# Kernel tuning notes

Hardware: AMD Instinct MI355X
Metric: run time of the kernel (lower is better)

The kernel has to match this reference:

```python
import jax, jax.numpy as jnp
import numpy as np

# ---- static part graph (matches torch.nonzero row-major edge order) ----
ADJ = np.array([[0,1,0,0,0,0],
                [1,0,1,1,1,1],
                [0,1,0,0,0,0],
                [0,1,0,0,0,0],
                [0,1,0,0,0,1],
                [0,1,0,0,1,0]], dtype=np.int64)
EDGES = [(int(u), int(v)) for u, v in np.argwhere(ADJ)]  # 12 edges
P = ADJ.shape[0]                 # 6 part nodes (cls_p - 1)
PART_LIST = [[] for _ in range(P)]
for u, v in EDGES:
    PART_LIST[v].append(u)
DEG = [len(l) for l in PART_LIST]  # [1,5,1,1,2,2], sum = 12
CLS_P = P + 1
IN_DIM, HID = 256, 10
N, H, W = 4, 64, 64


def spatial_coords(h, w):
    """[8,h,w] coord features, same as generate_spatial_batch (vectorized)."""
    ws = np.arange(w, dtype=np.float32); hs = np.arange(h, dtype=np.float32)
    xmin = ws / w * 2 - 1; xmax = (ws + 1) / w * 2 - 1; xctr = (xmin + xmax) / 2
    ymin = hs / h * 2 - 1; ymax = (hs + 1) / h * 2 - 1; yctr = (ymin + ymax) / 2
    f = np.zeros((h, w, 8), np.float32)
    f[..., 0] = xmin[None, :]; f[..., 1] = ymin[:, None]
    f[..., 2] = xmax[None, :]; f[..., 3] = ymax[:, None]
    f[..., 4] = xctr[None, :]; f[..., 5] = yctr[:, None]
    f[..., 6] = 1.0 / w;       f[..., 7] = 1.0 / h
    return jnp.asarray(f.transpose(2, 0, 1))


def conv1x1(x, w, b=None):
    y = jnp.einsum('nchw,oc->nohw', x, w)
    return y if b is None else y + b[None, :, None, None]


def conv3x3(x, w):
    return jax.lax.conv_general_dilated(x, w, (1, 1), 'SAME',
                                        dimension_numbers=('NCHW', 'OIHW', 'NCHW'))


def bn(x, g, b, eps=1e-5):
    mu = x.mean((0, 2, 3), keepdims=True)
    var = ((x - mu) ** 2).mean((0, 2, 3), keepdims=True)
    return (x - mu) * jax.lax.rsqrt(var + eps) * g[None, :, None, None] + b[None, :, None, None]


def setup_inputs() -> dict:
    key = jax.random.key(0)
    ks = jax.random.split(key, 16)
    s = 0.05
    return {
        'xp':      jax.random.normal(ks[0], (N, IN_DIM, H, W), jnp.float32),
        'p_nodes': jax.random.normal(ks[1], (CLS_P, N, HID, H, W), jnp.float32),
        'p_atts':  jax.random.normal(ks[2], (CLS_P, N, 1, H, W), jnp.float32),
        'W_key':  jax.random.normal(ks[3], (64, IN_DIM + 8), jnp.float32) * s,
        'b_key':  jnp.zeros((64,), jnp.float32),
        'W_q':    jax.random.normal(ks[4], (64, IN_DIM + 8), jnp.float32) * s,
        'b_q':    jnp.zeros((64,), jnp.float32),
        'W_att':  jax.random.normal(ks[5], (sum(DEG), IN_DIM + 1), jnp.float32) * s,
        'b_att':  jnp.zeros((sum(DEG),), jnp.float32),
        'W_proj': jax.random.normal(ks[6], (HID, IN_DIM), jnp.float32) * s,
        'g_proj': jnp.ones((HID,), jnp.float32),
        'bt_proj': jnp.zeros((HID,), jnp.float32),
        'W_rel1': jax.random.normal(ks[7], (2 * HID, 2 * HID, 3, 3), jnp.float32) * s,
        'g_rel1': jnp.ones((2 * HID,), jnp.float32),
        'bt_rel1': jnp.zeros((2 * HID,), jnp.float32),
        'W_rel2': jax.random.normal(ks[8], (HID, 2 * HID), jnp.float32) * s,
        'b_rel2': jnp.zeros((HID,), jnp.float32),
        'Wg':    jax.random.normal(ks[9], (P, 2, 2 * HID), jnp.float32) * s,
        'bg':    jnp.zeros((P, 2), jnp.float32),
        'Wc':    jax.random.normal(ks[10], (P, HID, 2 * HID), jnp.float32) * s,
        'g_can': jnp.ones((P, HID), jnp.float32),
        'bt_can': jnp.zeros((P, HID), jnp.float32),
    }


def reference(xp, p_nodes, p_atts,
              W_key, b_key, W_q, b_q, W_att, b_att,
              W_proj, g_proj, bt_proj, W_rel1, g_rel1, bt_rel1, W_rel2, b_rel2,
              Wg, bg, Wc, g_can, bt_can):
    n, c, h, w = xp.shape
    L = h * w
    coord = jnp.broadcast_to(spatial_coords(h, w), (n, 8, h, w))

    # ---- Dep_Context (vectorized over the P part nodes) ----
    feat = jnp.concatenate([xp, coord], axis=1)                 # [n, 264, h, w]
    key_f = conv1x1(feat, W_key, b_key).reshape(n, 64, L)       # [n, 64, L]
    p_att = p_atts[1:]                                          # [P, n, 1, h, w]
    norm = jax.nn.softmax(p_att.reshape(P, n, L), axis=-1)      # [P, n, L]
    hu_c = jnp.einsum('ncl,pnl->pnc', xp.reshape(n, c, L), norm)       # [P, n, 256]
    co_c = jnp.einsum('ncl,pnl->pnc', coord.reshape(n, 8, L), norm)    # [P, n, 8]
    cen = jnp.concatenate([hu_c, co_c], axis=-1)                # [P, n, 264]
    q = jnp.einsum('pnf,of->pno', cen, W_q) + b_q               # [P, n, 64]
    energy = jnp.einsum('pno,nol->pnl', q, key_f)               # [P, n, L]
    attn = jax.nn.sigmoid(energy).reshape(P, n, 1, h, w)
    one_m = 1.0 - p_att
    F_dep_att = attn * one_m                                    # [P, n, 1, h, w]
    F_dep = attn * xp[None] * one_m                             # [P, n, 256, h, w]

    # ---- Contexture attention heads (per-node conv, deg_i output channels) ----
    att_logits, att_soft = [], []
    off = 0
    for i in range(P):
        d = DEG[i]
        inp = jnp.concatenate([F_dep_att[i], xp], axis=1)       # [n, 257, h, w]
        logit = conv1x1(inp, W_att[off:off + d], b_att[off:off + d])
        att_logits.append(logit)
        att_soft.append(jax.nn.softmax(logit, axis=1))
        off += d

    # ---- Dependency messages per edge ----
    def dependency(hv, hu_ctx, dep_att):
        msg = jax.nn.relu(bn(conv1x1(hu_ctx * dep_att, W_proj), g_proj, bt_proj))
        x = jnp.concatenate([msg, hv], axis=1)                  # [n, 20, h, w]
        x = jax.nn.relu(bn(conv3x3(x, W_rel1), g_rel1, bt_rel1))
        return jax.nn.sigmoid(conv1x1(x, W_rel2, b_rel2))       # [n, 10, h, w]

    msgs = [None] * P
    for u, v in EDGES:
        ch = PART_LIST[u].index(v)
        # NB: original code indexes p_node_list with the raw edge target v
        m = dependency(p_nodes[v], F_dep[u], att_soft[u][:, ch:ch + 1])
        msgs[v] = m if msgs[v] is None else msgs[v] + m

    # ---- ConvGRU node updates ----
    new_nodes = [p_nodes[0]]
    for i in range(P):
        h_cur, msg = p_nodes[i + 1], msgs[i]
        gates = conv1x1(jnp.concatenate([msg, h_cur], axis=1), Wg[i], bg[i])
        r = jax.nn.sigmoid(gates[:, 0:1]); z = jax.nn.sigmoid(gates[:, 1:2])
        cnm = conv1x1(jnp.concatenate([msg, r * h_cur], axis=1), Wc[i])
        cnm = jax.nn.leaky_relu(bn(cnm, g_can[i], bt_can[i]), 0.01)  # InPlaceABNSync default
        new_nodes.append((1.0 - z) * h_cur + z * cnm)

    xp_new = jnp.stack(new_nodes)                               # [cls_p, n, 10, h, w]
    fdep_att = jnp.concatenate(att_logits, axis=1)              # [n, 12, h, w]
    return xp_new, fdep_att
```

## Files before the change

### kernel.cpp

```cpp
#include <hip/hip_runtime.h>
#include <math.h>

#define L 4096

__constant__ int c_EV[12]   = {1,0,2,3,4,5,1,1,1,5,1,4};
__constant__ int c_INOFF[7] = {0,1,6,7,8,10,12};
__constant__ int c_INE[12]  = {1, 0,6,7,8,10, 2, 3, 4,11, 5,9};

__device__ inline float sigmf(float x){ return 1.f/(1.f+expf(-x)); }

__global__ __launch_bounds__(256) void k_softmax_norm(const float* __restrict__ p_atts,
                                                      float* __restrict__ norm,
                                                      const float* __restrict__ W_rel1,
                                                      float* __restrict__ wt2){
  int tid = threadIdx.x;
  if (blockIdx.x == 24){
    for (int i = tid; i < 3600; i += 256){
      int co = i % 10; int t = i / 10;
      int k = t % 9; t /= 9;
      int h = t & 1; int ci = t >> 1;
      wt2[i] = W_rel1[(((h * 10 + co) * 20) + ci) * 9 + k];
    }
    return;
  }
  int pn = blockIdx.x;
  const float* src = p_atts + (size_t)(pn + 4) * L;
  float* dst = norm + (size_t)pn * L;
  __shared__ float red[256];
  float m = -1e30f;
  for (int l = tid; l < L; l += 256) m = fmaxf(m, src[l]);
  red[tid] = m; __syncthreads();
  for (int s = 128; s; s >>= 1){ if (tid < s) red[tid] = fmaxf(red[tid], red[tid+s]); __syncthreads(); }
  m = red[0]; __syncthreads();
  float sum = 0.f;
  for (int l = tid; l < L; l += 256) sum += expf(src[l] - m);
  red[tid] = sum; __syncthreads();
  for (int s = 128; s; s >>= 1){ if (tid < s) red[tid] += red[tid+s]; __syncthreads(); }
  float inv = 1.f / red[0];
  for (int l = tid; l < L; l += 256) dst[l] = expf(src[l] - m) * inv;
}

__device__ inline float coord_feat(int cc, int l){
  int h = l >> 6, w = l & 63;
  const float s = 2.f / 64.f;
  switch (cc){
    case 0: return w * s - 1.f;
    case 1: return h * s - 1.f;
    case 2: return (w + 1) * s - 1.f;
    case 3: return (h + 1) * s - 1.f;
    case 4: return (w + 0.5f) * s - 1.f;
    case 5: return (h + 0.5f) * s - 1.f;
    default: return 1.f / 64.f;
  }
}

__global__ __launch_bounds__(256) void k_centroid(const float* __restrict__ xp,
                                                  const float* __restrict__ norm,
                                                  float* __restrict__ cen){
  int c0 = blockIdx.x;
  int c1 = c0 + 132;
  int n = blockIdx.y;
  int tid = threadIdx.x;
  float acc[2][6];
#pragma unroll
  for (int q = 0; q < 2; q++)
#pragma unroll
    for (int p = 0; p < 6; p++) acc[q][p] = 0.f;
  const float* nr0 = norm + (size_t)n * L;
  const float* xr0 = xp + ((size_t)n * 256 + c0) * L;
  const float* xr1 = (c1 < 256) ? xp + ((size_t)n * 256 + c1) * L : nullptr;
  int cc1 = c1 - 256;
  for (int l = tid; l < L; l += 256){
    float nv[6];
#pragma unroll
    for (int p = 0; p < 6; p++) nv[p] = nr0[(size_t)p * 4 * L + l];
    float x0 = xr0[l];
    float x1 = (c1 < 256) ? xr1[l] : coord_feat(cc1, l);
#pragma unroll
    for (int p = 0; p < 6; p++){
      acc[0][p] = fmaf(x0, nv[p], acc[0][p]);
      acc[1][p] = fmaf(x1, nv[p], acc[1][p]);
    }
  }
#pragma unroll
  for (int q = 0; q < 2; q++)
#pragma unroll
    for (int p = 0; p < 6; p++){
      for (int off = 32; off; off >>= 1) acc[q][p] += __shfl_xor(acc[q][p], off, 64);
    }
  __shared__ float red[2][6][4];
  int wv = tid >> 6;
  if ((tid & 63) == 0){
#pragma unroll
    for (int q = 0; q < 2; q++)
#pragma unroll
      for (int p = 0; p < 6; p++) red[q][p][wv] = acc[q][p];
  }
  __syncthreads();
  if (tid < 12){
    int q = tid / 6, p = tid % 6;
    float s = red[q][p][0] + red[q][p][1] + red[q][p][2] + red[q][p][3];
    cen[(size_t)(p * 4 + n) * 264 + (q ? c1 : c0)] = s;
  }
}

__global__ __launch_bounds__(256) void k_qk(const float* __restrict__ cen,
                                            const float* __restrict__ W_q, const float* __restrict__ b_q,
                                            const float* __restrict__ W_key, const float* __restrict__ b_key,
                                            float* __restrict__ qk, float* __restrict__ qb){
  int pn = blockIdx.x;
  int tid = threadIdx.x;
  __shared__ float cen_s[264];
  __shared__ float qs[64];
  __shared__ float part[256];
  for (int i = tid; i < 264; i += 256) cen_s[i] = cen[(size_t)pn * 264 + i];
  __syncthreads();
  int o = tid >> 2, pr = tid & 3;
  {
    float a = 0.f;
    int f0 = pr * 66;
    for (int j = 0; j < 66; j++){ int f = f0 + j; a = fmaf(cen_s[f], W_q[o * 264 + f], a); }
    part[tid] = a;
  }
  __syncthreads();
  if (pr == 0) qs[o] = part[tid] + part[tid + 1] + part[tid + 2] + part[tid + 3] + b_q[o];
  __syncthreads();
  for (int c = tid; c < 264; c += 256){
    float a = 0.f;
    for (int oo = 0; oo < 64; oo++) a = fmaf(qs[oo], W_key[oo * 264 + c], a);
    qk[(size_t)pn * 264 + c] = a;
  }
  if (tid < 64) part[tid] = qs[tid] * b_key[tid];
  __syncthreads();
  if (tid == 0){
    float a = 0.f;
    for (int oo = 0; oo < 64; oo++) a += part[oo];
    qb[pn] = a;
  }
}

__global__ __launch_bounds__(256) void k_pixel(const float* __restrict__ xp,
                                              const float* __restrict__ p_atts,
                                              const float* __restrict__ W_att, const float* __restrict__ b_att,
                                              const float* __restrict__ W_proj,
                                              const float* __restrict__ qk, const float* __restrict__ qb,
                                              float* __restrict__ out_fdep,
                                              float* __restrict__ s_edge,
                                              float* __restrict__ proj_x,
                                              float* __restrict__ mpart){
  __shared__ float s_watt[256 * 12];
  __shared__ float s_wproj[256 * 12];
  __shared__ float s_qk[256 * 8];
  __shared__ float s_qkt[48];
  __shared__ float pacc[4][28][64];
  __shared__ float w0[12], ba[12], qbs[6];
  int n = blockIdx.y;
  int tid = threadIdx.x;
  int wv = tid >> 6, w = tid & 63;
  int l = blockIdx.x * 64 + w;
  for (int i = tid; i < 256 * 12; i += 256){ int c = i / 12, j = i % 12; s_watt[i] = W_att[j * 257 + 1 + c]; }
  for (int i = tid; i < 256 * 12; i += 256){ int c = i / 12, k = i % 12; s_wproj[i] = (k < 10) ? W_proj[k * 256 + c] : 0.f; }
  for (int i = tid; i < 256 * 8; i += 256){ int c = i >> 3, p = i & 7; s_qk[i] = (p < 6) ? qk[((size_t)(p * 4 + n)) * 264 + c] : 0.f; }
  if (tid < 48){ int p = tid >> 3, cc = tid & 7; s_qkt[tid] = qk[((size_t)(p * 4 + n)) * 264 + 256 + cc]; }
  if (tid < 12){ w0[tid] = W_att[tid * 257]; ba[tid] = b_att[tid]; }
  if (tid < 6) qbs[tid] = qb[tid * 4 + n];
  __syncthreads();

  float a[32];
#pragma unroll
  for (int f = 0; f < 32; f++) a[f] = 0.f;
  const float* xpn = xp + (size_t)n * 256 * L + l;
  int c0 = wv * 64;
#pragma unroll 2
  for (int cc = 0; cc < 64; cc++){
    int c = c0 + cc;
    float xv = xpn[(size_t)c * L];
    float4 wa0 = *(const float4*)(s_watt + c * 12);
    float4 wa1 = *(const float4*)(s_watt + c * 12 + 4);
    float4 wa2 = *(const float4*)(s_watt + c * 12 + 8);
    float4 wp0 = *(const float4*)(s_wproj + c * 12);
    float4 wp1 = *(const float4*)(s_wproj + c * 12 + 4);
    float4 wp2 = *(const float4*)(s_wproj + c * 12 + 8);
    float4 wq0 = *(const float4*)(s_qk + c * 8);
    float4 wq1 = *(const float4*)(s_qk + c * 8 + 4);
    a[0]  = fmaf(xv, wa0.x, a[0]);  a[1]  = fmaf(xv, wa0.y, a[1]);
    a[2]  = fmaf(xv, wa0.z, a[2]);  a[3]  = fmaf(xv, wa0.w, a[3]);
    a[4]  = fmaf(xv, wa1.x, a[4]);  a[5]  = fmaf(xv, wa1.y, a[5]);
    a[6]  = fmaf(xv, wa1.z, a[6]);  a[7]  = fmaf(xv, wa1.w, a[7]);
    a[8]  = fmaf(xv, wa2.x, a[8]);  a[9]  = fmaf(xv, wa2.y, a[9]);
    a[10] = fmaf(xv, wa2.z, a[10]); a[11] = fmaf(xv, wa2.w, a[11]);
    a[12] = fmaf(xv, wp0.x, a[12]); a[13] = fmaf(xv, wp0.y, a[13]);
    a[14] = fmaf(xv, wp0.z, a[14]); a[15] = fmaf(xv, wp0.w, a[15]);
    a[16] = fmaf(xv, wp1.x, a[16]); a[17] = fmaf(xv, wp1.y, a[17]);
    a[18] = fmaf(xv, wp1.z, a[18]); a[19] = fmaf(xv, wp1.w, a[19]);
    a[20] = fmaf(xv, wp2.x, a[20]); a[21] = fmaf(xv, wp2.y, a[21]);
    a[24] = fmaf(xv, wq0.x, a[24]); a[25] = fmaf(xv, wq0.y, a[25]);
    a[26] = fmaf(xv, wq0.z, a[26]); a[27] = fmaf(xv, wq0.w, a[27]);
    a[28] = fmaf(xv, wq1.x, a[28]); a[29] = fmaf(xv, wq1.y, a[29]);
  }
#pragma unroll
  for (int f = 0; f < 12; f++) pacc[wv][f][w] = a[f];
#pragma unroll
  for (int k = 0; k < 10; k++) pacc[wv][12 + k][w] = a[12 + k];
#pragma unroll
  for (int p = 0; p < 6; p++) pacc[wv][22 + p][w] = a[24 + p];
  __syncthreads();
  for (int idx = tid; idx < 28 * 64; idx += 256){
    int f = idx >> 6, ww = idx & 63;
    pacc[0][f][ww] = pacc[0][f][ww] + pacc[1][f][ww] + pacc[2][f][ww] + pacc[3][f][ww];
  }
  __syncthreads();
  float* se_lds = &pacc[1][0][0];
  if (tid < 64){
    float accA[12], accP[10], accE[6];
#pragma unroll
    for (int j = 0; j < 12; j++) accA[j] = pacc[0][j][w];
#pragma unroll
    for (int k = 0; k < 10; k++) accP[k] = pacc[0][12 + k][w];
#pragma unroll
    for (int p = 0; p < 6; p++) accE[p] = pacc[0][22 + p][w];

    float cf[8];
    { int hh = l >> 6, ww2 = l & 63; const float s = 2.f / 64.f;
      cf[0] = ww2 * s - 1.f; cf[1] = hh * s - 1.f; cf[2] = (ww2 + 1) * s - 1.f; cf[3] = (hh + 1) * s - 1.f;
      cf[4] = (ww2 + 0.5f) * s - 1.f; cf[5] = (hh + 0.5f) * s - 1.f; cf[6] = 1.f / 64.f; cf[7] = 1.f / 64.f; }
    float sat[6];
#pragma unroll
    for (int p = 0; p < 6; p++){
      float e = accE[p] + qbs[p];
#pragma unroll
      for (int cc = 0; cc < 8; cc++) e = fmaf(cf[cc], s_qkt[p * 8 + cc], e);
      float aa = sigmf(e);
      float pa = p_atts[((size_t)(p + 1) * 4 + n) * L + l];
      sat[p] = aa * (1.f - pa);
    }
    const int part_of[12] = {0,1,1,1,1,1,2,3,4,4,5,5};
    float lg[12];
#pragma unroll
    for (int j = 0; j < 12; j++){
      lg[j] = accA[j] + w0[j] * sat[part_of[j]] + ba[j];
      out_fdep[((size_t)n * 12 + j) * L + l] = lg[j];
    }
    const int gs[6] = {0,1,6,7,8,10}, gd[6] = {1,5,1,1,2,2};
    float sm[12];
#pragma unroll
    for (int g = 0; g < 6; g++){
      int s0 = gs[g], d = gd[g];
      float mx = lg[s0];
      for (int t = 1; t < d; t++) mx = fmaxf(mx, lg[s0 + t]);
      float ssum = 0.f;
      for (int t = 0; t < d; t++){ float e2 = expf(lg[s0 + t] - mx); sm[s0 + t] = e2; ssum += e2; }
      float inv = 1.f / ssum;
      for (int t = 0; t < d; t++) sm[s0 + t] *= inv;
    }
#pragma unroll
    for (int e = 0; e < 12; e++){
      float sev = sat[part_of[e]] * sm[e];
      s_edge[((size_t)e * 4 + n) * L + l] = sev;
      se_lds[e * 64 + w] = sev;
    }
#pragma unroll
    for (int k = 0; k < 10; k++) proj_x[((size_t)n * 10 + k) * L + l] = accP[k];
  }
  __syncthreads();
  {
    int blk = n * 64 + blockIdx.x;
#pragma unroll
    for (int j = 0; j < 30; j++){
      int pair = wv * 30 + j;
      int e = pair / 10, k = pair % 10;
      float t = se_lds[e * 64 + w] * pacc[0][12 + k][w];
      float s1 = t, s2 = t * t;
      for (int off = 32; off; off >>= 1){ s1 += __shfl_xor(s1, off, 64); s2 += __shfl_xor(s2, off, 64); }
      if (w == 0){
        mpart[((size_t)pair * 256 + blk) * 2]     = s1;
        mpart[((size_t)pair * 256 + blk) * 2 + 1] = s2;
      }
    }
  }
}

__global__ __launch_bounds__(256) void k_red256(const float* __restrict__ part,
                                                float* __restrict__ mu, float* __restrict__ istd){
  int ent = blockIdx.x;
  int t = threadIdx.x;
  const float* p = part + ((size_t)ent * 256 + t) * 2;
  float s1 = p[0], s2 = p[1];
  for (int off = 32; off; off >>= 1){ s1 += __shfl_xor(s1, off, 64); s2 += __shfl_xor(s2, off, 64); }
  __shared__ float r1[4], r2[4];
  if ((t & 63) == 0){ r1[t >> 6] = s1; r2[t >> 6] = s2; }
  __syncthreads();
  if (t == 0){
    float a1 = r1[0] + r1[1] + r1[2] + r1[3];
    float a2 = r2[0] + r2[1] + r2[2] + r2[3];
    float m = a1 / 16384.f, v = a2 / 16384.f - m * m;
    mu[ent] = m; istd[ent] = rsqrtf(v + 1e-5f);
  }
}

__global__ __launch_bounds__(256) void k_conv3(const float* __restrict__ proj_x,
                                               const float* __restrict__ s_edge,
                                               const float* __restrict__ mu, const float* __restrict__ istd,
                                               const float* __restrict__ g_proj, const float* __restrict__ bt_proj,
                                               const float* __restrict__ p_nodes,
                                               const float* __restrict__ wt2,
                                               float* __restrict__ y,
                                               float* __restrict__ ypart){
  __shared__ float red[4][20];
  int rb = blockIdx.x, n = blockIdx.y;
  int e = blockIdx.z >> 1, h = blockIdx.z & 1;
  int v = c_EV[e];
  int tid = threadIdx.x;
  int wv = tid >> 6, w = tid & 63;
  int r0 = rb * 8 + wv * 2;
  float mLm = (w == 0) ? 0.f : 1.f;
  float mRm = (w == 63) ? 0.f : 1.f;

  float scs[10], sbs[10];
#pragma unroll
  for (int k = 0; k < 10; k++){
    int ek = e * 10 + k;
    float s = istd[ek] * g_proj[k];
    scs[k] = s; sbs[k] = bt_proj[k] - mu[ek] * s;
  }
  const size_t enL = ((size_t)e * 4 + n) * L;
  const float* se = s_edge + enL;
  float se4[4];
#pragma unroll
  for (int j = 0; j < 4; j++){
    int rr = r0 - 1 + j;
    se4[j] = (rr >= 0 && rr < 64) ? se[rr * 64 + w] : 0.f;
  }

  float acc0[10], acc1[10];
#pragma unroll
  for (int co = 0; co < 10; co++){ acc0[co] = 0.f; acc1[co] = 0.f; }

  for (int ci = 0; ci < 10; ci++){
    const float* pr = proj_x + ((size_t)n * 10 + ci) * L;
    float mC[4];
#pragma unroll
    for (int j = 0; j < 4; j++){
      int rr = r0 - 1 + j;
      if (rr >= 0 && rr < 64){
        float t = pr[rr * 64 + w] * se4[j];
        mC[j] = fmaxf(fmaf(t, scs[ci], sbs[ci]), 0.f);
      } else mC[j] = 0.f;
    }
    float mL[4], mR[4];
#pragma unroll
    for (int j = 0; j < 4; j++){
      mL[j] = __shfl_up(mC[j], 1) * mLm;
      mR[j] = __shfl_down(mC[j], 1) * mRm;
    }
    const float* wp = wt2 + (ci * 2 + h) * 90;
#pragma unroll
    for (int ky = 0; ky < 3; ky++){
#pragma unroll
      for (int co = 0; co < 10; co++){
        float w0v = wp[(ky * 3 + 0) * 10 + co];
        float w1v = wp[(ky * 3 + 1) * 10 + co];
        float w2v = wp[(ky * 3 + 2) * 10 + co];
        acc0[co] = fmaf(mL[ky], w0v, fmaf(mC[ky], w1v, fmaf(mR[ky], w2v, acc0[co])));
        acc1[co] = fmaf(mL[ky + 1], w0v, fmaf(mC[ky + 1], w1v, fmaf(mR[ky + 1], w2v, acc1[co])));
      }
    }
  }
  for (int ci = 10; ci < 20; ci++){
    const float* pnp = p_nodes + (((size_t)v * 4 + n) * 10 + (ci - 10)) * L;
    float mC[4];
#pragma unroll
    for (int j = 0; j < 4; j++){
      int rr = r0 - 1 + j;
      mC[j] = (rr >= 0 && rr < 64) ? pnp[rr * 64 + w] : 0.f;
    }
    float mL[4], mR[4];
#pragma unroll
    for (int j = 0; j < 4; j++){
      mL[j] = __shfl_up(mC[j], 1) * mLm;
      mR[j] = __shfl_down(mC[j], 1) * mRm;
    }
    const float* wp = wt2 + (ci * 2 + h) * 90;
#pragma unroll
    for (int ky = 0; ky < 3; ky++){
#pragma unroll
      for (int co = 0; co < 10; co++){
        float w0v = wp[(ky * 3 + 0) * 10 + co];
        float w1v = wp[(ky * 3 + 1) * 10 + co];
        float w2v = wp[(ky * 3 + 2) * 10 + co];
        acc0[co] = fmaf(mL[ky], w0v, fmaf(mC[ky], w1v, fmaf(mR[ky], w2v, acc0[co])));
        acc1[co] = fmaf(mL[ky + 1], w0v, fmaf(mC[ky + 1], w1v, fmaf(mR[ky + 1], w2v, acc1[co])));
      }
    }
  }

  int ch0 = h * 10;
#pragma unroll
  for (int co = 0; co < 10; co++){
    size_t base = enL * 20 + ((size_t)(ch0 + co)) * L;
    y[base + r0 * 64 + w] = acc0[co];
    y[base + (r0 + 1) * 64 + w] = acc1[co];
  }

#pragma unroll
  for (int co = 0; co < 10; co++){
    float s1 = acc0[co] + acc1[co];
    float s2 = acc0[co] * acc0[co] + acc1[co] * acc1[co];
    for (int off = 32; off; off >>= 1){ s1 += __shfl_xor(s1, off, 64); s2 += __shfl_xor(s2, off, 64); }
    if (w == 0){ red[wv][2 * co] = s1; red[wv][2 * co + 1] = s2; }
  }
  __syncthreads();
  if (tid < 20){
    int co = tid >> 1, which = tid & 1;
    float s = red[0][tid] + red[1][tid] + red[2][tid] + red[3][tid];
    ypart[(((size_t)(e * 20 + ch0 + co) * 32) + n * 8 + rb) * 2 + which] = s;
  }
}

__global__ __launch_bounds__(64) void k_red(const float* __restrict__ part, int npart,
                                            float* __restrict__ mu, float* __restrict__ istd){
  int ent = blockIdx.x;
  int t = threadIdx.x;
  float s1 = 0.f, s2 = 0.f;
  if (t < npart){
    const float* p = part + ((size_t)ent * npart + t) * 2;
    s1 = p[0]; s2 = p[1];
  }
  for (int off = 32; off; off >>= 1){ s1 += __shfl_xor(s1, off, 64); s2 += __shfl_xor(s2, off, 64); }
  if (t == 0){
    float m = s1 / 16384.f, v = s2 / 16384.f - m * m;
    mu[ent] = m; istd[ent] = rsqrtf(v + 1e-5f);
  }
}

__global__ __launch_bounds__(256) void k_mout_gru(const float* __restrict__ y,
                                                  const float* __restrict__ mu_y, const float* __restrict__ istd_y,
                                                  const float* __restrict__ g_rel1, const float* __restrict__ bt_rel1,
                                                  const float* __restrict__ W_rel2, const float* __restrict__ b_rel2,
                                                  const float* __restrict__ p_nodes,
                                                  const float* __restrict__ Wg, const float* __restrict__ bg,
                                                  const float* __restrict__ Wc,
                                                  float* __restrict__ cnm, float* __restrict__ zbuf,
                                                  float* __restrict__ cpart){
  int i = blockIdx.z, n = blockIdx.y;
  int tid = threadIdx.x;
  int l = blockIdx.x * 256 + tid;
  __shared__ float w2[200], wc[200], wg[40], bgs[2];
  __shared__ float sc[5][20], sb[5][20];
  __shared__ float red[4][20];
  int ne = c_INOFF[i + 1] - c_INOFF[i];
  for (int t = tid; t < 200; t += 256){ w2[t] = W_rel2[t]; wc[t] = Wc[i * 200 + t]; }
  if (tid < 40) wg[tid] = Wg[i * 40 + tid];
  if (tid < 2) bgs[tid] = bg[i * 2 + tid];
  if (tid < ne * 20){
    int ei = tid / 20, c = tid % 20;
    int e = c_INE[c_INOFF[i] + ei];
    int ec = e * 20 + c;
    float s = istd_y[ec] * g_rel1[c];
    sc[ei][c] = s; sb[ei][c] = bt_rel1[c] - mu_y[ec] * s;
  }
  __syncthreads();
  float m[10];
#pragma unroll
  for (int k = 0; k < 10; k++) m[k] = 0.f;
  for (int ei = 0; ei < ne; ei++){
    int e = c_INE[c_INOFF[i] + ei];
    float z[20];
#pragma unroll
    for (int c = 0; c < 20; c++){
      float t = y[(((size_t)e * 4 + n) * 20 + c) * L + l];
      z[c] = fmaxf(t * sc[ei][c] + sb[ei][c], 0.f);
    }
#pragma unroll
    for (int k = 0; k < 10; k++){
      float a = b_rel2[k];
#pragma unroll
      for (int c = 0; c < 20; c++) a = fmaf(w2[k * 20 + c], z[c], a);
      m[k] += sigmf(a);
    }
  }
  float h[10];
#pragma unroll
  for (int k = 0; k < 10; k++) h[k] = p_nodes[(((size_t)(i + 1) * 4 + n) * 10 + k) * L + l];
  float g0 = bgs[0], g1 = bgs[1];
#pragma unroll
  for (int k = 0; k < 10; k++){
    g0 = fmaf(wg[k], m[k], g0); g0 = fmaf(wg[10 + k], h[k], g0);
    g1 = fmaf(wg[20 + k], m[k], g1); g1 = fmaf(wg[30 + k], h[k], g1);
  }
  float r = sigmf(g0), zz = sigmf(g1);
  zbuf[((size_t)i * 4 + n) * L + l] = zz;
  float cv[10];
#pragma unroll
  for (int k = 0; k < 10; k++){
    float a = 0.f;
#pragma unroll
    for (int c = 0; c < 10; c++){
      a = fmaf(wc[k * 20 + c], m[c], a);
      a = fmaf(wc[k * 20 + 10 + c], r * h[c], a);
    }
    cv[k] = a;
    cnm[(((size_t)i * 4 + n) * 10 + k) * L + l] = a;
  }
  int wv = tid >> 6, w = tid & 63;
#pragma unroll
  for (int k = 0; k < 10; k++){
    float s1 = cv[k], s2 = cv[k] * cv[k];
    for (int off = 32; off; off >>= 1){ s1 += __shfl_xor(s1, off, 64); s2 += __shfl_xor(s2, off, 64); }
    if (w == 0){ red[wv][2 * k] = s1; red[wv][2 * k + 1] = s2; }
  }
  __syncthreads();
  if (tid < 20){
    float s = red[0][tid] + red[1][tid] + red[2][tid] + red[3][tid];
    int k = tid >> 1, which = tid & 1;
    cpart[(((size_t)(i * 10 + k) * 64) + n * 16 + blockIdx.x) * 2 + which] = s;
  }
}

__global__ __launch_bounds__(256) void k_out(const float* __restrict__ cnm, const float* __restrict__ zbuf,
                                             const float* __restrict__ p_nodes,
                                             const float* __restrict__ mu, const float* __restrict__ istd,
                                             const float* __restrict__ g_can, const float* __restrict__ bt_can,
                                             float* __restrict__ out){
  int idx = blockIdx.x * 256 + threadIdx.x;
  const int NODE = 4 * 10 * L;
  if (idx < NODE){ out[idx] = p_nodes[idx]; return; }
  int j = idx - NODE;
  int l = j & (L - 1); int r = j >> 12;
  int k = r % 10; r /= 10; int n = r & 3; int i = r >> 2;
  int ik = i * 10 + k;
  float c = cnm[j];
  float cn = (c - mu[ik]) * istd[ik] * g_can[ik] + bt_can[ik];
  cn = cn > 0.f ? cn : 0.01f * cn;
  float z = zbuf[((size_t)i * 4 + n) * L + l];
  float h = p_nodes[idx];
  out[idx] = (1.f - z) * h + z * cn;
}

extern "C" void kernel_launch(void* const* d_in, const int* in_sizes, int n_in,
                              void* d_out, int out_size, void* d_ws, size_t ws_size,
                              hipStream_t stream){
  (void)in_sizes; (void)n_in; (void)out_size; (void)ws_size;
  const float* xp      = (const float*)d_in[0];
  const float* p_nodes = (const float*)d_in[1];
  const float* p_atts  = (const float*)d_in[2];
  const float* W_key   = (const float*)d_in[3];
  const float* b_key   = (const float*)d_in[4];
  const float* W_q     = (const float*)d_in[5];
  const float* b_q     = (const float*)d_in[6];
  const float* W_att   = (const float*)d_in[7];
  const float* b_att   = (const float*)d_in[8];
  const float* W_proj  = (const float*)d_in[9];
  const float* g_proj  = (const float*)d_in[10];
  const float* bt_proj = (const float*)d_in[11];
  const float* W_rel1  = (const float*)d_in[12];
  const float* g_rel1  = (const float*)d_in[13];
  const float* bt_rel1 = (const float*)d_in[14];
  const float* W_rel2  = (const float*)d_in[15];
  const float* b_rel2  = (const float*)d_in[16];
  const float* Wg      = (const float*)d_in[17];
  const float* bg      = (const float*)d_in[18];
  const float* Wc      = (const float*)d_in[19];
  const float* g_can   = (const float*)d_in[20];
  const float* bt_can  = (const float*)d_in[21];

  float* out      = (float*)d_out;
  float* fdep_out = out + (size_t)7 * 4 * 10 * L;

  float* w = (float*)d_ws;
  size_t off = 0;
  auto alloc = [&](size_t nf){ float* p = w + off; off += nf; return p; };
  float* norm    = alloc((size_t)6 * 4 * L);
  float* cen     = alloc(6 * 4 * 264);
  float* qk      = alloc(6 * 4 * 264);
  float* qb      = alloc(24);
  float* wt2     = alloc(3600);
  float* proj_x  = alloc((size_t)4 * 10 * L);
  float* s_edge  = alloc((size_t)12 * 4 * L);
  float* mpart   = alloc(120 * 256 * 2);
  float* mu_msg  = alloc(120);
  float* istd_msg= alloc(120);
  float* ybuf    = alloc((size_t)12 * 4 * 20 * L);
  float* ypart   = alloc(240 * 32 * 2);
  float* cpart   = alloc(60 * 64 * 2);
  float* mu_y    = alloc(240);
  float* istd_y  = alloc(240);
  float* cnm     = alloc((size_t)6 * 4 * 10 * L);
  float* zbuf    = alloc((size_t)6 * 4 * L);
  float* mu_c    = alloc(60);
  float* istd_c  = alloc(60);

  k_softmax_norm<<<25, 256, 0, stream>>>(p_atts, norm, W_rel1, wt2);
  { dim3 g(132, 4); k_centroid<<<g, 256, 0, stream>>>(xp, norm, cen); }
  k_qk<<<24, 256, 0, stream>>>(cen, W_q, b_q, W_key, b_key, qk, qb);
  { dim3 g(64, 4); k_pixel<<<g, 256, 0, stream>>>(xp, p_atts, W_att, b_att, W_proj, qk, qb, fdep_out, s_edge, proj_x, mpart); }
  k_red256<<<120, 256, 0, stream>>>(mpart, mu_msg, istd_msg);
  { dim3 g(8, 4, 24); k_conv3<<<g, 256, 0, stream>>>(proj_x, s_edge, mu_msg, istd_msg, g_proj, bt_proj, p_nodes, wt2, ybuf, ypart); }
  k_red<<<240, 64, 0, stream>>>(ypart, 32, mu_y, istd_y);
  { dim3 g(16, 4, 6); k_mout_gru<<<g, 256, 0, stream>>>(ybuf, mu_y, istd_y, g_rel1, bt_rel1, W_rel2, b_rel2,
                                                        p_nodes, Wg, bg, Wc, cnm, zbuf, cpart); }
  k_red<<<60, 64, 0, stream>>>(cpart, 64, mu_c, istd_c);
  k_out<<<(7 * 4 * 10 * L) / 256, 256, 0, stream>>>(cnm, zbuf, p_nodes, mu_c, istd_c, g_can, bt_can, out);
}
```

Before: 144.7 us.

## Split message computation per edge from GRU kernel and batch pixel loads

The fused message+GRU kernel is split into a per-edge kernel (12 edges in parallel) that writes sigmoid messages to a new buffer, and a GRU kernel that sums incoming edge messages. This removes the load imbalance where node 1 processed five edges serially while others did one. In the pixel kernel, four channel loads of xp are issued ahead of the FMA block to raise memory-level parallelism. The split adds an extra launch and a round-trip of a 12x4x10xL intermediate through global memory.

```diff
diff --git a/kernel.cpp b/kernel.cpp
--- a/kernel.cpp
+++ b/kernel.cpp
@@ -171,32 +171,37 @@
   for (int f = 0; f < 32; f++) a[f] = 0.f;
   const float* xpn = xp + (size_t)n * 256 * L + l;
   int c0 = wv * 64;
-#pragma unroll 2
-  for (int cc = 0; cc < 64; cc++){
-    int c = c0 + cc;
-    float xv = xpn[(size_t)c * L];
-    float4 wa0 = *(const float4*)(s_watt + c * 12);
-    float4 wa1 = *(const float4*)(s_watt + c * 12 + 4);
-    float4 wa2 = *(const float4*)(s_watt + c * 12 + 8);
-    float4 wp0 = *(const float4*)(s_wproj + c * 12);
-    float4 wp1 = *(const float4*)(s_wproj + c * 12 + 4);
-    float4 wp2 = *(const float4*)(s_wproj + c * 12 + 8);
-    float4 wq0 = *(const float4*)(s_qk + c * 8);
-    float4 wq1 = *(const float4*)(s_qk + c * 8 + 4);
-    a[0]  = fmaf(xv, wa0.x, a[0]);  a[1]  = fmaf(xv, wa0.y, a[1]);
-    a[2]  = fmaf(xv, wa0.z, a[2]);  a[3]  = fmaf(xv, wa0.w, a[3]);
-    a[4]  = fmaf(xv, wa1.x, a[4]);  a[5]  = fmaf(xv, wa1.y, a[5]);
-    a[6]  = fmaf(xv, wa1.z, a[6]);  a[7]  = fmaf(xv, wa1.w, a[7]);
-    a[8]  = fmaf(xv, wa2.x, a[8]);  a[9]  = fmaf(xv, wa2.y, a[9]);
-    a[10] = fmaf(xv, wa2.z, a[10]); a[11] = fmaf(xv, wa2.w, a[11]);
-    a[12] = fmaf(xv, wp0.x, a[12]); a[13] = fmaf(xv, wp0.y, a[13]);
-    a[14] = fmaf(xv, wp0.z, a[14]); a[15] = fmaf(xv, wp0.w, a[15]);
-    a[16] = fmaf(xv, wp1.x, a[16]); a[17] = fmaf(xv, wp1.y, a[17]);
-    a[18] = fmaf(xv, wp1.z, a[18]); a[19] = fmaf(xv, wp1.w, a[19]);
-    a[20] = fmaf(xv, wp2.x, a[20]); a[21] = fmaf(xv, wp2.y, a[21]);
-    a[24] = fmaf(xv, wq0.x, a[24]); a[25] = fmaf(xv, wq0.y, a[25]);
-    a[26] = fmaf(xv, wq0.z, a[26]); a[27] = fmaf(xv, wq0.w, a[27]);
-    a[28] = fmaf(xv, wq1.x, a[28]); a[29] = fmaf(xv, wq1.y, a[29]);
+  for (int cc = 0; cc < 64; cc += 4){
+    float xv4[4];
+#pragma unroll
+    for (int u = 0; u < 4; u++) xv4[u] = xpn[(size_t)(c0 + cc + u) * L];
+#pragma unroll
+    for (int u = 0; u < 4; u++){
+      int c = c0 + cc + u;
+      float xv = xv4[u];
+      float4 wa0 = *(const float4*)(s_watt + c * 12);
+      float4 wa1 = *(const float4*)(s_watt + c * 12 + 4);
+      float4 wa2 = *(const float4*)(s_watt + c * 12 + 8);
+      float4 wp0 = *(const float4*)(s_wproj + c * 12);
+      float4 wp1 = *(const float4*)(s_wproj + c * 12 + 4);
+      float4 wp2 = *(const float4*)(s_wproj + c * 12 + 8);
+      float4 wq0 = *(const float4*)(s_qk + c * 8);
+      float4 wq1 = *(const float4*)(s_qk + c * 8 + 4);
+      a[0]  = fmaf(xv, wa0.x, a[0]);  a[1]  = fmaf(xv, wa0.y, a[1]);
+      a[2]  = fmaf(xv, wa0.z, a[2]);  a[3]  = fmaf(xv, wa0.w, a[3]);
+      a[4]  = fmaf(xv, wa1.x, a[4]);  a[5]  = fmaf(xv, wa1.y, a[5]);
+      a[6]  = fmaf(xv, wa1.z, a[6]);  a[7]  = fmaf(xv, wa1.w, a[7]);
+      a[8]  = fmaf(xv, wa2.x, a[8]);  a[9]  = fmaf(xv, wa2.y, a[9]);
+      a[10] = fmaf(xv, wa2.z, a[10]); a[11] = fmaf(xv, wa2.w, a[11]);
+      a[12] = fmaf(xv, wp0.x, a[12]); a[13] = fmaf(xv, wp0.y, a[13]);
+      a[14] = fmaf(xv, wp0.z, a[14]); a[15] = fmaf(xv, wp0.w, a[15]);
+      a[16] = fmaf(xv, wp1.x, a[16]); a[17] = fmaf(xv, wp1.y, a[17]);
+      a[18] = fmaf(xv, wp1.z, a[18]); a[19] = fmaf(xv, wp1.w, a[19]);
+      a[20] = fmaf(xv, wp2.x, a[20]); a[21] = fmaf(xv, wp2.y, a[21]);
+      a[24] = fmaf(xv, wq0.x, a[24]); a[25] = fmaf(xv, wq0.y, a[25]);
+      a[26] = fmaf(xv, wq0.z, a[26]); a[27] = fmaf(xv, wq0.w, a[27]);
+      a[28] = fmaf(xv, wq1.x, a[28]); a[29] = fmaf(xv, wq1.y, a[29]);
+    }
   }
 #pragma unroll
   for (int f = 0; f < 12; f++) pacc[wv][f][w] = a[f];
@@ -433,51 +438,60 @@
   }
 }
 
-__global__ __launch_bounds__(256) void k_mout_gru(const float* __restrict__ y,
-                                                  const float* __restrict__ mu_y, const float* __restrict__ istd_y,
-                                                  const float* __restrict__ g_rel1, const float* __restrict__ bt_rel1,
-                                                  const float* __restrict__ W_rel2, const float* __restrict__ b_rel2,
-                                                  const float* __restrict__ p_nodes,
-                                                  const float* __restrict__ Wg, const float* __restrict__ bg,
-                                                  const float* __restrict__ Wc,
-                                                  float* __restrict__ cnm, float* __restrict__ zbuf,
-                                                  float* __restrict__ cpart){
+__global__ __launch_bounds__(256) void k_mout(const float* __restrict__ y,
+                                              const float* __restrict__ mu_y, const float* __restrict__ istd_y,
+                                              const float* __restrict__ g_rel1, const float* __restrict__ bt_rel1,
+                                              const float* __restrict__ W_rel2, const float* __restrict__ b_rel2,
+                                              float* __restrict__ m_out){
+  int e = blockIdx.z, n = blockIdx.y;
+  int l = blockIdx.x * 256 + threadIdx.x;
+  __shared__ float w2[200], sc[20], sb[20];
+  for (int i = threadIdx.x; i < 200; i += 256) w2[i] = W_rel2[i];
+  if (threadIdx.x < 20){
+    int c = threadIdx.x; int ec = e * 20 + c;
+    float s = istd_y[ec] * g_rel1[c];
+    sc[c] = s; sb[c] = bt_rel1[c] - mu_y[ec] * s;
+  }
+  __syncthreads();
+  float z[20];
+#pragma unroll
+  for (int c = 0; c < 20; c++){
+    float t = y[(((size_t)e * 4 + n) * 20 + c) * L + l];
+    z[c] = fmaxf(t * sc[c] + sb[c], 0.f);
+  }
+#pragma unroll
+  for (int k = 0; k < 10; k++){
+    float a = b_rel2[k];
+#pragma unroll
+    for (int c = 0; c < 20; c++) a = fmaf(w2[k * 20 + c], z[c], a);
+    m_out[(((size_t)e * 4 + n) * 10 + k) * L + l] = sigmf(a);
+  }
+}
+
+__global__ __launch_bounds__(256) void k_gru(const float* __restrict__ m_out,
+                                             const float* __restrict__ p_nodes,
+                                             const float* __restrict__ Wg, const float* __restrict__ bg,
+                                             const float* __restrict__ Wc,
+                                             float* __restrict__ cnm, float* __restrict__ zbuf,
+                                             float* __restrict__ cpart){
   int i = blockIdx.z, n = blockIdx.y;
   int tid = threadIdx.x;
   int l = blockIdx.x * 256 + tid;
-  __shared__ float w2[200], wc[200], wg[40], bgs[2];
-  __shared__ float sc[5][20], sb[5][20];
+  __shared__ float wc[200], wg[40], bgs[2];
   __shared__ float red[4][20];
-  int ne = c_INOFF[i + 1] - c_INOFF[i];
-  for (int t = tid; t < 200; t += 256){ w2[t] = W_rel2[t]; wc[t] = Wc[i * 200 + t]; }
+  for (int t = tid; t < 200; t += 256) wc[t] = Wc[i * 200 + t];
   if (tid < 40) wg[tid] = Wg[i * 40 + tid];
   if (tid < 2) bgs[tid] = bg[i * 2 + tid];
-  if (tid < ne * 20){
-    int ei = tid / 20, c = tid % 20;
-    int e = c_INE[c_INOFF[i] + ei];
-    int ec = e * 20 + c;
-    float s = istd_y[ec] * g_rel1[c];
-    sc[ei][c] = s; sb[ei][c] = bt_rel1[c] - mu_y[ec] * s;
-  }
   __syncthreads();
   float m[10];
 #pragma unroll
-  for (int k = 0; k < 10; k++) m[k] = 0.f;
-  for (int ei = 0; ei < ne; ei++){
-    int e = c_INE[c_INOFF[i] + ei];
-    float z[20];
-#pragma unroll
-    for (int c = 0; c < 20; c++){
-      float t = y[(((size_t)e * 4 + n) * 20 + c) * L + l];
-      z[c] = fmaxf(t * sc[ei][c] + sb[ei][c], 0.f);
-    }
-#pragma unroll
-    for (int k = 0; k < 10; k++){
-      float a = b_rel2[k];
-#pragma unroll
-      for (int c = 0; c < 20; c++) a = fmaf(w2[k * 20 + c], z[c], a);
-      m[k] += sigmf(a);
-    }
+  for (int k = 0; k < 10; k++){
+    float a = 0.f;
+    for (int t = c_INOFF[i]; t < c_INOFF[i + 1]; t++){
+      int e = c_INE[t];
+      a += m_out[(((size_t)e * 4 + n) * 10 + k) * L + l];
+    }
+    m[k] = a;
   }
   float h[10];
 #pragma unroll
@@ -585,6 +599,7 @@
   float* cpart   = alloc(60 * 64 * 2);
   float* mu_y    = alloc(240);
   float* istd_y  = alloc(240);
+  float* m_out   = alloc((size_t)12 * 4 * 10 * L);
   float* cnm     = alloc((size_t)6 * 4 * 10 * L);
   float* zbuf    = alloc((size_t)6 * 4 * L);
   float* mu_c    = alloc(60);
@@ -597,8 +612,8 @@
   k_red256<<<120, 256, 0, stream>>>(mpart, mu_msg, istd_msg);
   { dim3 g(8, 4, 24); k_conv3<<<g, 256, 0, stream>>>(proj_x, s_edge, mu_msg, istd_msg, g_proj, bt_proj, p_nodes, wt2, ybuf, ypart); }
   k_red<<<240, 64, 0, stream>>>(ypart, 32, mu_y, istd_y);
-  { dim3 g(16, 4, 6); k_mout_gru<<<g, 256, 0, stream>>>(ybuf, mu_y, istd_y, g_rel1, bt_rel1, W_rel2, b_rel2,
-                                                        p_nodes, Wg, bg, Wc, cnm, zbuf, cpart); }
+  { dim3 g(16, 4, 12); k_mout<<<g, 256, 0, stream>>>(ybuf, mu_y, istd_y, g_rel1, bt_rel1, W_rel2, b_rel2, m_out); }
+  { dim3 g(16, 4, 6); k_gru<<<g, 256, 0, stream>>>(m_out, p_nodes, Wg, bg, Wc, cnm, zbuf, cpart); }
   k_red<<<60, 64, 0, stream>>>(cpart, 64, mu_c, istd_c);
   k_out<<<(7 * 4 * 10 * L) / 256, 256, 0, stream>>>(cnm, zbuf, p_nodes, mu_c, istd_c, g_can, bt_can, out);
 }
```

Result: slower. 149.1 us (+3.0%).
